# Optimization experiments

Hardware: AMD Instinct MI355X
Metric: run time of the kernel (lower is better)

## Reference

```python
import jax, jax.numpy as jnp
import numpy as np

B, C, H, W = 32, 1024, 28, 28
TEXT_DIM = 768
ATTN_DIM = 256
REDUCTION = 16
RED = max(1, C // REDUCTION)


def setup_inputs() -> dict:
    key = jax.random.key(0)
    ks = jax.random.split(key, 8)
    x = jax.random.normal(ks[0], (B, C, H, W), dtype=jnp.float32)
    text_feat = jax.random.normal(ks[1], (B, TEXT_DIM), dtype=jnp.float32)
    # ChannelAttention shared MLP (Linear weights, torch layout [out, in], no bias)
    w1 = jax.random.normal(ks[2], (RED, C), dtype=jnp.float32) * (1.0 / np.sqrt(C))
    w2 = jax.random.normal(ks[3], (C, RED), dtype=jnp.float32) * (1.0 / np.sqrt(RED))
    # TextGuidedSpatialAttention projections
    wq = jax.random.normal(ks[4], (ATTN_DIM, TEXT_DIM), dtype=jnp.float32) * 0.001
    wk = jax.random.normal(ks[5], (ATTN_DIM, C), dtype=jnp.float32) * np.sqrt(2.0 / ATTN_DIM)
    wv = jax.random.normal(ks[6], (ATTN_DIM, C), dtype=jnp.float32) * np.sqrt(2.0 / ATTN_DIM)
    wo = jax.random.normal(ks[7], (1, ATTN_DIM), dtype=jnp.float32) * np.sqrt(2.0)
    return {"x": x, "text_feat": text_feat, "w1": w1, "w2": w2,
            "wq": wq, "wk": wk, "wv": wv, "wo": wo}


def _forward(x, text_feat, w1, w2, wq, wk, wv, wo):
    b, c, h, w = x.shape
    # ----- Channel attention -----
    avg = jnp.mean(x, axis=(2, 3))          # [B, C]
    mx = jnp.max(x, axis=(2, 3))            # [B, C]
    def mlp(z):
        return jax.nn.relu(z @ w1.T) @ w2.T  # [B, C]
    ch_attn = jax.nn.sigmoid(mlp(avg) + mlp(mx))   # [B, C]
    x = x * ch_attn[:, :, None, None]
    # ----- Text-guided spatial attention -----
    q = text_feat @ wq.T                     # [B, A]
    # 1x1 conv == channel contraction
    k = jnp.einsum('ac,bchw->bahw', wk, x).reshape(b, ATTN_DIM, h * w)  # [B, A, N]
    v = jnp.einsum('ac,bchw->bahw', wv, x).reshape(b, ATTN_DIM, h * w)  # [B, A, N]
    scores = jnp.einsum('ba,ban->bn', q, k) / jnp.sqrt(jnp.float32(ATTN_DIM))  # [B, N]
    attn_weights = jax.nn.softmax(scores, axis=-1)                      # [B, N]
    attended = jnp.einsum('bn,ban->ba', attn_weights, v)                # [B, A]
    # out_proj 1x1 conv on a spatially-constant tensor == scalar per batch, broadcast
    spatial_scalar = jax.nn.sigmoid(attended @ wo.T)                    # [B, 1]
    spatial_attn = jnp.broadcast_to(spatial_scalar[:, :, None, None], (b, 1, h, w))
    return x * spatial_attn, spatial_attn


def reference(x, text_feat, w1, w2, wq, wk, wv, wo):
    return _forward(x, text_feat, w1, w2, wq, wk, wv, wo)
```

## Files before the change

kernel.cpp:

```cpp
#include <hip/hip_runtime.h>
#include <math.h>

#define B_   32
#define C_   1024
#define N_   784
#define NF4  196
#define TD   768
#define AD   256
#define RED_ 64
#define OUT0 25690112
#define ROWS (B_*C_)
#define SCH  16

#define OFF_AVG  0
#define OFF_MAX  32768
#define OFF_CA   65536
#define OFF_Q    98304
#define OFF_HS   106496
#define OFF_G    108544
#define OFF_WVO  141312
#define OFF_ATTN 142336
#define OFF_T    167424
#define OFF_S    200192
#define OFF_PART 200224

__global__ void k_avgmax(const float* __restrict__ x, float* __restrict__ avg,
                         float* __restrict__ mx) {
    int row  = blockIdx.x * 4 + (threadIdx.x >> 6);
    int lane = threadIdx.x & 63;
    const float4* xr = (const float4*)(x + (size_t)row * N_);
    float s = 0.f, m = -3.4e38f;
    for (int i = lane; i < NF4; i += 64) {
        float4 v = xr[i];
        s += v.x + v.y + v.z + v.w;
        m = fmaxf(m, fmaxf(fmaxf(v.x, v.y), fmaxf(v.z, v.w)));
    }
    for (int o = 32; o; o >>= 1) {
        s += __shfl_down(s, o, 64);
        m = fmaxf(m, __shfl_down(m, o, 64));
    }
    if (lane == 0) { avg[row] = s * (1.f / (float)N_); mx[row] = m; }
}

__global__ void k_q(const float* __restrict__ text, const float* __restrict__ wq,
                    float* __restrict__ q) {
    int w    = blockIdx.x * 4 + (threadIdx.x >> 6);
    int lane = threadIdx.x & 63;
    int b = w >> 8, a = w & 255;
    const float4* tb = (const float4*)(text + (size_t)b * TD);
    const float4* wr = (const float4*)(wq + (size_t)a * TD);
    float acc = 0.f;
    #pragma unroll
    for (int j = 0; j < 3; ++j) {
        int i = lane + 64 * j;
        float4 tv = tb[i], wv = wr[i];
        acc += tv.x * wv.x + tv.y * wv.y + tv.z * wv.z + tv.w * wv.w;
    }
    for (int o = 32; o; o >>= 1) acc += __shfl_down(acc, o, 64);
    if (lane == 0) q[(size_t)b * AD + a] = acc;
}

__global__ void k_wvo(const float* __restrict__ wv, const float* __restrict__ wo,
                      float* __restrict__ wvo) {
    int c = blockIdx.x * 256 + threadIdx.x;
    float acc = 0.f;
    for (int a = 0; a < AD; ++a) acc += wo[a] * wv[(size_t)a * C_ + c];
    wvo[c] = acc;
}

__global__ void k_h(const float* __restrict__ avg, const float* __restrict__ mx,
                    const float* __restrict__ w1, float* __restrict__ hs) {
    int w    = blockIdx.x * 4 + (threadIdx.x >> 6);
    int lane = threadIdx.x & 63;
    int b = w >> 6, r = w & 63;
    const float4* av = (const float4*)(avg + (size_t)b * C_);
    const float4* mv = (const float4*)(mx + (size_t)b * C_);
    const float4* wr = (const float4*)(w1 + (size_t)r * C_);
    float aa = 0.f, am = 0.f;
    #pragma unroll
    for (int j = 0; j < 4; ++j) {
        int i = lane + 64 * j;
        float4 wv = wr[i], a4 = av[i], m4 = mv[i];
        aa += wv.x * a4.x + wv.y * a4.y + wv.z * a4.z + wv.w * a4.w;
        am += wv.x * m4.x + wv.y * m4.y + wv.z * m4.z + wv.w * m4.w;
    }
    for (int o = 32; o; o >>= 1) {
        aa += __shfl_down(aa, o, 64);
        am += __shfl_down(am, o, 64);
    }
    if (lane == 0) hs[(size_t)b * RED_ + r] = fmaxf(aa, 0.f) + fmaxf(am, 0.f);
}

__global__ void k_ca(const float* __restrict__ hs, const float* __restrict__ w2,
                     float* __restrict__ ca) {
    int w    = blockIdx.x * 4 + (threadIdx.x >> 6);
    int lane = threadIdx.x & 63;
    int b = w >> 10, c = w & 1023;
    float p = hs[(size_t)b * RED_ + lane] * w2[(size_t)c * RED_ + lane];
    for (int o = 32; o; o >>= 1) p += __shfl_down(p, o, 64);
    if (lane == 0) ca[(size_t)b * C_ + c] = 1.f / (1.f + __expf(-p));
}

__global__ void k_g(const float* __restrict__ q, const float* __restrict__ wk,
                    const float* __restrict__ ca, float* __restrict__ g) {
    int b = blockIdx.y;
    int c = blockIdx.x * 256 + threadIdx.x;
    __shared__ float qs[AD];
    if (threadIdx.x < AD) qs[threadIdx.x] = q[(size_t)b * AD + threadIdx.x];
    __syncthreads();
    float acc = 0.f;
    for (int a = 0; a < AD; ++a) acc += qs[a] * wk[(size_t)a * C_ + c];
    g[(size_t)b * C_ + c] = acc * ca[(size_t)b * C_ + c] * 0.0625f;
}

__global__ void k_scores(const float* __restrict__ x, const float* __restrict__ g,
                         float* __restrict__ part) {
    int chunk = blockIdx.x;
    int b     = blockIdx.y;
    int t     = threadIdx.x;
    int wave  = t >> 6, lane = t & 63;
    __shared__ float gs[64];
    __shared__ float lred[4 * NF4 * 4];
    if (t < 64) gs[t] = g[(size_t)b * C_ + chunk * 64 + t];
    __syncthreads();
    const float4* xb4 = (const float4*)(x +
        ((size_t)b * C_ + (size_t)chunk * 64 + (size_t)wave * 16) * N_);
    float4 a0 = {0,0,0,0}, a1 = {0,0,0,0}, a2 = {0,0,0,0}, a3 = {0,0,0,0};
    #pragma unroll
    for (int c = 0; c < 16; ++c) {
        float gv = gs[wave * 16 + c];
        const float4* row = xb4 + (size_t)c * NF4;
        float4 v;
        v = row[lane];       a0.x += gv*v.x; a0.y += gv*v.y; a0.z += gv*v.z; a0.w += gv*v.w;
        v = row[lane + 64];  a1.x += gv*v.x; a1.y += gv*v.y; a1.z += gv*v.z; a1.w += gv*v.w;
        v = row[lane + 128]; a2.x += gv*v.x; a2.y += gv*v.y; a2.z += gv*v.z; a2.w += gv*v.w;
        if (lane < 4) {
            v = row[lane + 192]; a3.x += gv*v.x; a3.y += gv*v.y; a3.z += gv*v.z; a3.w += gv*v.w;
        }
    }
    float4* l4 = (float4*)lred;
    l4[wave * NF4 + lane]       = a0;
    l4[wave * NF4 + lane + 64]  = a1;
    l4[wave * NF4 + lane + 128] = a2;
    if (lane < 4) l4[wave * NF4 + lane + 192] = a3;
    __syncthreads();
    if (t < NF4) {
        float4 s0 = l4[t], s1 = l4[NF4 + t], s2 = l4[2 * NF4 + t], s3 = l4[3 * NF4 + t];
        float4 r;
        r.x = s0.x + s1.x + s2.x + s3.x;
        r.y = s0.y + s1.y + s2.y + s3.y;
        r.z = s0.z + s1.z + s2.z + s3.z;
        r.w = s0.w + s1.w + s2.w + s3.w;
        ((float4*)(part + ((size_t)b * SCH + chunk) * N_))[t] = r;
    }
}

__global__ void k_softmax(const float* __restrict__ part, float* __restrict__ attn) {
    int b = blockIdx.x;
    int t = threadIdx.x;
    int lane = t & 63, wave = t >> 6;
    const float* p = part + (size_t)b * SCH * N_;
    float v0 = 0.f, v1 = 0.f, v2 = 0.f, v3 = 0.f;
    for (int ch = 0; ch < SCH; ++ch) {
        const float* pc = p + (size_t)ch * N_;
        v0 += pc[t]; v1 += pc[t + 256]; v2 += pc[t + 512];
        if (t < 16) v3 += pc[t + 768];
    }
    float m = fmaxf(fmaxf(v0, v1), v2);
    if (t < 16) m = fmaxf(m, v3);
    for (int o = 32; o; o >>= 1) m = fmaxf(m, __shfl_down(m, o, 64));
    __shared__ float rm[4], rs[4];
    if (lane == 0) rm[wave] = m;
    __syncthreads();
    float M = fmaxf(fmaxf(rm[0], rm[1]), fmaxf(rm[2], rm[3]));
    float e0 = __expf(v0 - M), e1 = __expf(v1 - M), e2 = __expf(v2 - M);
    float e3 = (t < 16) ? __expf(v3 - M) : 0.f;
    float ssum = e0 + e1 + e2 + e3;
    for (int o = 32; o; o >>= 1) ssum += __shfl_down(ssum, o, 64);
    if (lane == 0) rs[wave] = ssum;
    __syncthreads();
    float inv = 1.f / (rs[0] + rs[1] + rs[2] + rs[3]);
    float* ab = attn + (size_t)b * N_;
    ab[t] = e0 * inv; ab[t + 256] = e1 * inv; ab[t + 512] = e2 * inv;
    if (t < 16) ab[t + 768] = e3 * inv;
}

__global__ void k_attend(const float* __restrict__ x, const float* __restrict__ attn,
                         const float* __restrict__ chattn, float* __restrict__ t_out) {
    int row  = blockIdx.x * 4 + (threadIdx.x >> 6);
    int lane = threadIdx.x & 63;
    int b    = row >> 10;
    const float4* xr = (const float4*)(x + (size_t)row * N_);
    const float4* ar = (const float4*)(attn + (size_t)b * N_);
    float s = 0.f;
    for (int i = lane; i < NF4; i += 64) {
        float4 xv = xr[i]; float4 av = ar[i];
        s += xv.x * av.x + xv.y * av.y + xv.z * av.z + xv.w * av.w;
    }
    for (int o = 32; o; o >>= 1) s += __shfl_down(s, o, 64);
    if (lane == 0) t_out[row] = s * chattn[row];
}

__global__ void k_scalar(const float* __restrict__ wvo, const float* __restrict__ t_in,
                         float* __restrict__ s_out) {
    int b    = blockIdx.x * 4 + (threadIdx.x >> 6);
    int lane = threadIdx.x & 63;
    const float4* tb = (const float4*)(t_in + (size_t)b * C_);
    const float4* wv = (const float4*)wvo;
    float acc = 0.f;
    #pragma unroll
    for (int j = 0; j < 4; ++j) {
        int i = lane + 64 * j;
        float4 tv = tb[i], wvv = wv[i];
        acc += tv.x * wvv.x + tv.y * wvv.y + tv.z * wvv.z + tv.w * wvv.w;
    }
    for (int o = 32; o; o >>= 1) acc += __shfl_down(acc, o, 64);
    if (lane == 0) s_out[b] = 1.f / (1.f + __expf(-acc));
}

__global__ void k_finalize(const float* __restrict__ x, const float* __restrict__ chattn,
                           const float* __restrict__ s, float* __restrict__ out) {
    int blk = blockIdx.x;
    if (blk < ROWS / 4) {
        int row  = blk * 4 + (threadIdx.x >> 6);
        int lane = threadIdx.x & 63;
        float sc = chattn[row] * s[row >> 10];
        const float4* xr = (const float4*)(x + (size_t)row * N_);
        float4* orow = (float4*)(out + (size_t)row * N_);
        for (int i = lane; i < NF4; i += 64) {
            float4 v = xr[i];
            v.x *= sc; v.y *= sc; v.z *= sc; v.w *= sc;
            orow[i] = v;
        }
    } else {
        int idx = (blk - ROWS / 4) * 256 + threadIdx.x;
        if (idx < (B_ * N_) / 4) {
            int b = idx / (N_ / 4);
            float v = s[b];
            ((float4*)(out + OUT0))[idx] = make_float4(v, v, v, v);
        }
    }
}

extern "C" void kernel_launch(void* const* d_in, const int* in_sizes, int n_in,
                              void* d_out, int out_size, void* d_ws, size_t ws_size,
                              hipStream_t stream) {
    const float* x    = (const float*)d_in[0];
    const float* text = (const float*)d_in[1];
    const float* w1   = (const float*)d_in[2];
    const float* w2   = (const float*)d_in[3];
    const float* wq   = (const float*)d_in[4];
    const float* wk   = (const float*)d_in[5];
    const float* wv   = (const float*)d_in[6];
    const float* wo   = (const float*)d_in[7];
    float* out = (float*)d_out;
    float* ws  = (float*)d_ws;

    float* avg  = ws + OFF_AVG;
    float* mx   = ws + OFF_MAX;
    float* ca   = ws + OFF_CA;
    float* q    = ws + OFF_Q;
    float* hs   = ws + OFF_HS;
    float* g    = ws + OFF_G;
    float* wvo  = ws + OFF_WVO;
    float* attn = ws + OFF_ATTN;
    float* tt   = ws + OFF_T;
    float* sv   = ws + OFF_S;
    float* part = ws + OFF_PART;

    k_avgmax<<<ROWS / 4, 256, 0, stream>>>(x, avg, mx);
    k_q<<<(B_ * AD) / 4, 256, 0, stream>>>(text, wq, q);
    k_wvo<<<C_ / 256, 256, 0, stream>>>(wv, wo, wvo);
    k_h<<<(B_ * RED_) / 4, 256, 0, stream>>>(avg, mx, w1, hs);
    k_ca<<<(B_ * C_) / 4, 256, 0, stream>>>(hs, w2, ca);
    k_g<<<dim3(C_ / 256, B_), 256, 0, stream>>>(q, wk, ca, g);
    k_scores<<<dim3(SCH, B_), 256, 0, stream>>>(x, g, part);
    k_softmax<<<B_, 256, 0, stream>>>(part, attn);
    k_attend<<<ROWS / 4, 256, 0, stream>>>(x, attn, ca, tt);
    k_scalar<<<B_ / 4, 256, 0, stream>>>(wvo, tt, sv);
    k_finalize<<<ROWS / 4 + 25, 256, 0, stream>>>(x, ca, sv, out);
}
```

Measured before the change: 308.2 us.

## Fuse small projection kernels, widen score split, fold scalar into atomics

```diff
diff --git a/kernel.cpp b/kernel.cpp
--- a/kernel.cpp
+++ b/kernel.cpp
@@ -10,7 +10,7 @@
 #define RED_ 64
 #define OUT0 25690112
 #define ROWS (B_*C_)
-#define SCH  16
+#define SCH  64
 
 #define OFF_AVG  0
 #define OFF_MAX  32768
@@ -20,9 +20,8 @@
 #define OFF_G    108544
 #define OFF_WVO  141312
 #define OFF_ATTN 142336
-#define OFF_T    167424
-#define OFF_S    200192
-#define OFF_PART 200224
+#define OFF_SDOT 167424
+#define OFF_PART 167456
 
 __global__ void k_avgmax(const float* __restrict__ x, float* __restrict__ avg,
                          float* __restrict__ mx) {
@@ -42,75 +41,74 @@
     if (lane == 0) { avg[row] = s * (1.f / (float)N_); mx[row] = m; }
 }
 
-__global__ void k_q(const float* __restrict__ text, const float* __restrict__ wq,
-                    float* __restrict__ q) {
-    int w    = blockIdx.x * 4 + (threadIdx.x >> 6);
-    int lane = threadIdx.x & 63;
-    int b = w >> 8, a = w & 255;
-    const float4* tb = (const float4*)(text + (size_t)b * TD);
-    const float4* wr = (const float4*)(wq + (size_t)a * TD);
-    float acc = 0.f;
+__global__ void k_proj(const float* __restrict__ text, const float* __restrict__ wq,
+                       const float* __restrict__ avg, const float* __restrict__ mx,
+                       const float* __restrict__ w1, const float* __restrict__ wv,
+                       const float* __restrict__ wo, float* __restrict__ q,
+                       float* __restrict__ hs, float* __restrict__ wvo) {
+    int blk  = blockIdx.x;
+    int wave = threadIdx.x >> 6, lane = threadIdx.x & 63;
+    if (blk < 2048) {
+        int w = blk * 4 + wave;
+        int b = w >> 8, a = w & 255;
+        const float4* tb = (const float4*)(text + (size_t)b * TD);
+        const float4* wr = (const float4*)(wq + (size_t)a * TD);
+        float acc = 0.f;
+        #pragma unroll
+        for (int j = 0; j < 3; ++j) {
+            int i = lane + 64 * j;
+            float4 tv = tb[i], wvv = wr[i];
+            acc += tv.x * wvv.x + tv.y * wvv.y + tv.z * wvv.z + tv.w * wvv.w;
+        }
+        for (int o = 32; o; o >>= 1) acc += __shfl_down(acc, o, 64);
+        if (lane == 0) q[(size_t)b * AD + a] = acc;
+    } else if (blk < 2560) {
+        int w = (blk - 2048) * 4 + wave;
+        int b = w >> 6, r = w & 63;
+        const float4* av = (const float4*)(avg + (size_t)b * C_);
+        const float4* mv = (const float4*)(mx + (size_t)b * C_);
+        const float4* wr = (const float4*)(w1 + (size_t)r * C_);
+        float aa = 0.f, am = 0.f;
+        #pragma unroll
+        for (int j = 0; j < 4; ++j) {
+            int i = lane + 64 * j;
+            float4 wvv = wr[i], a4 = av[i], m4 = mv[i];
+            aa += wvv.x * a4.x + wvv.y * a4.y + wvv.z * a4.z + wvv.w * a4.w;
+            am += wvv.x * m4.x + wvv.y * m4.y + wvv.z * m4.z + wvv.w * m4.w;
+        }
+        for (int o = 32; o; o >>= 1) {
+            aa += __shfl_down(aa, o, 64);
+            am += __shfl_down(am, o, 64);
+        }
+        if (lane == 0) hs[(size_t)b * RED_ + r] = fmaxf(aa, 0.f) + fmaxf(am, 0.f);
+    } else {
+        int c = (blk - 2560) * 256 + threadIdx.x;
+        float acc = 0.f;
+        for (int a = 0; a < AD; ++a) acc += wo[a] * wv[(size_t)a * C_ + c];
+        wvo[c] = acc;
+    }
+}
+
+__global__ void k_cag(const float* __restrict__ hs, const float* __restrict__ w2,
+                      const float* __restrict__ q, const float* __restrict__ wk,
+                      float* __restrict__ ca, float* __restrict__ g) {
+    int b = blockIdx.y;
+    int t = threadIdx.x;
+    int c = blockIdx.x * 256 + t;
+    __shared__ float qs[AD];
+    __shared__ float hss[RED_];
+    qs[t] = q[(size_t)b * AD + t];
+    if (t < RED_) hss[t] = hs[(size_t)b * RED_ + t];
+    __syncthreads();
+    float a1 = 0.f;
     #pragma unroll
-    for (int j = 0; j < 3; ++j) {
-        int i = lane + 64 * j;
-        float4 tv = tb[i], wv = wr[i];
-        acc += tv.x * wv.x + tv.y * wv.y + tv.z * wv.z + tv.w * wv.w;
-    }
-    for (int o = 32; o; o >>= 1) acc += __shfl_down(acc, o, 64);
-    if (lane == 0) q[(size_t)b * AD + a] = acc;
-}
-
-__global__ void k_wvo(const float* __restrict__ wv, const float* __restrict__ wo,
-                      float* __restrict__ wvo) {
-    int c = blockIdx.x * 256 + threadIdx.x;
-    float acc = 0.f;
-    for (int a = 0; a < AD; ++a) acc += wo[a] * wv[(size_t)a * C_ + c];
-    wvo[c] = acc;
-}
-
-__global__ void k_h(const float* __restrict__ avg, const float* __restrict__ mx,
-                    const float* __restrict__ w1, float* __restrict__ hs) {
-    int w    = blockIdx.x * 4 + (threadIdx.x >> 6);
-    int lane = threadIdx.x & 63;
-    int b = w >> 6, r = w & 63;
-    const float4* av = (const float4*)(avg + (size_t)b * C_);
-    const float4* mv = (const float4*)(mx + (size_t)b * C_);
-    const float4* wr = (const float4*)(w1 + (size_t)r * C_);
-    float aa = 0.f, am = 0.f;
-    #pragma unroll
-    for (int j = 0; j < 4; ++j) {
-        int i = lane + 64 * j;
-        float4 wv = wr[i], a4 = av[i], m4 = mv[i];
-        aa += wv.x * a4.x + wv.y * a4.y + wv.z * a4.z + wv.w * a4.w;
-        am += wv.x * m4.x + wv.y * m4.y + wv.z * m4.z + wv.w * m4.w;
-    }
-    for (int o = 32; o; o >>= 1) {
-        aa += __shfl_down(aa, o, 64);
-        am += __shfl_down(am, o, 64);
-    }
-    if (lane == 0) hs[(size_t)b * RED_ + r] = fmaxf(aa, 0.f) + fmaxf(am, 0.f);
-}
-
-__global__ void k_ca(const float* __restrict__ hs, const float* __restrict__ w2,
-                     float* __restrict__ ca) {
-    int w    = blockIdx.x * 4 + (threadIdx.x >> 6);
-    int lane = threadIdx.x & 63;
-    int b = w >> 10, c = w & 1023;
-    float p = hs[(size_t)b * RED_ + lane] * w2[(size_t)c * RED_ + lane];
-    for (int o = 32; o; o >>= 1) p += __shfl_down(p, o, 64);
-    if (lane == 0) ca[(size_t)b * C_ + c] = 1.f / (1.f + __expf(-p));
-}
-
-__global__ void k_g(const float* __restrict__ q, const float* __restrict__ wk,
-                    const float* __restrict__ ca, float* __restrict__ g) {
-    int b = blockIdx.y;
-    int c = blockIdx.x * 256 + threadIdx.x;
-    __shared__ float qs[AD];
-    if (threadIdx.x < AD) qs[threadIdx.x] = q[(size_t)b * AD + threadIdx.x];
-    __syncthreads();
-    float acc = 0.f;
-    for (int a = 0; a < AD; ++a) acc += qs[a] * wk[(size_t)a * C_ + c];
-    g[(size_t)b * C_ + c] = acc * ca[(size_t)b * C_ + c] * 0.0625f;
+    for (int r = 0; r < RED_; ++r) a1 += hss[r] * w2[(size_t)c * RED_ + r];
+    float cav = 1.f / (1.f + __expf(-a1));
+    ca[(size_t)b * C_ + c] = cav;
+    float a2 = 0.f;
+    #pragma unroll 8
+    for (int a = 0; a < AD; ++a) a2 += qs[a] * wk[(size_t)a * C_ + c];
+    g[(size_t)b * C_ + c] = a2 * cav * 0.0625f;
 }
 
 __global__ void k_scores(const float* __restrict__ x, const float* __restrict__ g,
@@ -119,16 +117,16 @@
     int b     = blockIdx.y;
     int t     = threadIdx.x;
     int wave  = t >> 6, lane = t & 63;
-    __shared__ float gs[64];
-    __shared__ float lred[4 * NF4 * 4];
-    if (t < 64) gs[t] = g[(size_t)b * C_ + chunk * 64 + t];
+    __shared__ float gs[16];
+    __shared__ float4 l4[4 * NF4];
+    if (t < 16) gs[t] = g[(size_t)b * C_ + chunk * 16 + t];
     __syncthreads();
     const float4* xb4 = (const float4*)(x +
-        ((size_t)b * C_ + (size_t)chunk * 64 + (size_t)wave * 16) * N_);
+        ((size_t)b * C_ + (size_t)chunk * 16 + (size_t)wave * 4) * N_);
     float4 a0 = {0,0,0,0}, a1 = {0,0,0,0}, a2 = {0,0,0,0}, a3 = {0,0,0,0};
     #pragma unroll
-    for (int c = 0; c < 16; ++c) {
-        float gv = gs[wave * 16 + c];
+    for (int c = 0; c < 4; ++c) {
+        float gv = gs[wave * 4 + c];
         const float4* row = xb4 + (size_t)c * NF4;
         float4 v;
         v = row[lane];       a0.x += gv*v.x; a0.y += gv*v.y; a0.z += gv*v.z; a0.w += gv*v.w;
@@ -138,7 +136,6 @@
             v = row[lane + 192]; a3.x += gv*v.x; a3.y += gv*v.y; a3.z += gv*v.z; a3.w += gv*v.w;
         }
     }
-    float4* l4 = (float4*)lred;
     l4[wave * NF4 + lane]       = a0;
     l4[wave * NF4 + lane + 64]  = a1;
     l4[wave * NF4 + lane + 128] = a2;
@@ -155,10 +152,12 @@
     }
 }
 
-__global__ void k_softmax(const float* __restrict__ part, float* __restrict__ attn) {
+__global__ void k_softmax(const float* __restrict__ part, float* __restrict__ attn,
+                          float* __restrict__ sdot) {
     int b = blockIdx.x;
     int t = threadIdx.x;
     int lane = t & 63, wave = t >> 6;
+    if (t == 0) sdot[b] = 0.f;
     const float* p = part + (size_t)b * SCH * N_;
     float v0 = 0.f, v1 = 0.f, v2 = 0.f, v3 = 0.f;
     for (int ch = 0; ch < SCH; ++ch) {
@@ -186,45 +185,41 @@
 }
 
 __global__ void k_attend(const float* __restrict__ x, const float* __restrict__ attn,
-                         const float* __restrict__ chattn, float* __restrict__ t_out) {
-    int row  = blockIdx.x * 4 + (threadIdx.x >> 6);
-    int lane = threadIdx.x & 63;
-    int b    = row >> 10;
+                         const float* __restrict__ chattn, const float* __restrict__ wvo,
+                         float* __restrict__ sdot) {
+    int wave = threadIdx.x >> 6, lane = threadIdx.x & 63;
+    int row  = blockIdx.x * 4 + wave;
+    int b    = row >> 10, c = row & 1023;
     const float4* xr = (const float4*)(x + (size_t)row * N_);
     const float4* ar = (const float4*)(attn + (size_t)b * N_);
     float s = 0.f;
-    for (int i = lane; i < NF4; i += 64) {
-        float4 xv = xr[i]; float4 av = ar[i];
+    #pragma unroll
+    for (int j = 0; j < 3; ++j) {
+        int i = lane + 64 * j;
+        float4 xv = xr[i], av = ar[i];
         s += xv.x * av.x + xv.y * av.y + xv.z * av.z + xv.w * av.w;
     }
+    if (lane < 4) {
+        float4 xv = xr[lane + 192], av = ar[lane + 192];
+        s += xv.x * av.x + xv.y * av.y + xv.z * av.z + xv.w * av.w;
+    }
     for (int o = 32; o; o >>= 1) s += __shfl_down(s, o, 64);
-    if (lane == 0) t_out[row] = s * chattn[row];
-}
-
-__global__ void k_scalar(const float* __restrict__ wvo, const float* __restrict__ t_in,
-                         float* __restrict__ s_out) {
-    int b    = blockIdx.x * 4 + (threadIdx.x >> 6);
-    int lane = threadIdx.x & 63;
-    const float4* tb = (const float4*)(t_in + (size_t)b * C_);
-    const float4* wv = (const float4*)wvo;
-    float acc = 0.f;
-    #pragma unroll
-    for (int j = 0; j < 4; ++j) {
-        int i = lane + 64 * j;
-        float4 tv = tb[i], wvv = wv[i];
-        acc += tv.x * wvv.x + tv.y * wvv.y + tv.z * wvv.z + tv.w * wvv.w;
-    }
-    for (int o = 32; o; o >>= 1) acc += __shfl_down(acc, o, 64);
-    if (lane == 0) s_out[b] = 1.f / (1.f + __expf(-acc));
+    __shared__ float wsum[4];
+    if (lane == 0) wsum[wave] = s * chattn[row] * wvo[c];
+    __syncthreads();
+    if (threadIdx.x == 0)
+        atomicAdd(&sdot[b], wsum[0] + wsum[1] + wsum[2] + wsum[3]);
 }
 
 __global__ void k_finalize(const float* __restrict__ x, const float* __restrict__ chattn,
-                           const float* __restrict__ s, float* __restrict__ out) {
+                           const float* __restrict__ sdot, float* __restrict__ out) {
     int blk = blockIdx.x;
     if (blk < ROWS / 4) {
         int row  = blk * 4 + (threadIdx.x >> 6);
         int lane = threadIdx.x & 63;
-        float sc = chattn[row] * s[row >> 10];
+        int b    = row >> 10;
+        float sb = 1.f / (1.f + __expf(-sdot[b]));
+        float sc = chattn[row] * sb;
         const float4* xr = (const float4*)(x + (size_t)row * N_);
         float4* orow = (float4*)(out + (size_t)row * N_);
         for (int i = lane; i < NF4; i += 64) {
@@ -236,7 +231,7 @@
         int idx = (blk - ROWS / 4) * 256 + threadIdx.x;
         if (idx < (B_ * N_) / 4) {
             int b = idx / (N_ / 4);
-            float v = s[b];
+            float v = 1.f / (1.f + __expf(-sdot[b]));
             ((float4*)(out + OUT0))[idx] = make_float4(v, v, v, v);
         }
     }
@@ -264,19 +259,14 @@
     float* g    = ws + OFF_G;
     float* wvo  = ws + OFF_WVO;
     float* attn = ws + OFF_ATTN;
-    float* tt   = ws + OFF_T;
-    float* sv   = ws + OFF_S;
+    float* sdot = ws + OFF_SDOT;
     float* part = ws + OFF_PART;
 
     k_avgmax<<<ROWS / 4, 256, 0, stream>>>(x, avg, mx);
-    k_q<<<(B_ * AD) / 4, 256, 0, stream>>>(text, wq, q);
-    k_wvo<<<C_ / 256, 256, 0, stream>>>(wv, wo, wvo);
-    k_h<<<(B_ * RED_) / 4, 256, 0, stream>>>(avg, mx, w1, hs);
-    k_ca<<<(B_ * C_) / 4, 256, 0, stream>>>(hs, w2, ca);
-    k_g<<<dim3(C_ / 256, B_), 256, 0, stream>>>(q, wk, ca, g);
+    k_proj<<<2564, 256, 0, stream>>>(text, wq, avg, mx, w1, wv, wo, q, hs, wvo);
+    k_cag<<<dim3(C_ / 256, B_), 256, 0, stream>>>(hs, w2, q, wk, ca, g);
     k_scores<<<dim3(SCH, B_), 256, 0, stream>>>(x, g, part);
-    k_softmax<<<B_, 256, 0, stream>>>(part, attn);
-    k_attend<<<ROWS / 4, 256, 0, stream>>>(x, attn, ca, tt);
-    k_scalar<<<B_ / 4, 256, 0, stream>>>(wvo, tt, sv);
-    k_finalize<<<ROWS / 4 + 25, 256, 0, stream>>>(x, ca, sv, out);
-}
+    k_softmax<<<B_, 256, 0, stream>>>(part, attn, sdot);
+    k_attend<<<ROWS / 4, 256, 0, stream>>>(x, attn, ca, wvo, sdot);
+    k_finalize<<<ROWS / 4 + 25, 256, 0, stream>>>(x, ca, sdot, out);
+}
```

Result: slower. 373.5 us (+21.2%).
